# Kernel tuning notes

Hardware: AMD Instinct MI355X
Metric: run time of the kernel (lower is better)

The kernel has to match this reference:

```python
import jax, jax.numpy as jnp
import numpy as np

N_DYADIC = 0  # dyadic refinement order 'n' from SigLoss_MMD.__init__


def _sig_gram(X, Y, n):
    """Gram matrix of signature kernels k(x_i, y_j) via the first-order
    finite-difference PDE scheme used by sig_kernels_f/fb_mmd:
        K[i+1,j+1] = K[i+1,j] + K[i,j+1] + K[i,j]*(<dx_i, dy_j> - 1)
    with dyadically refined increments dx = (x_{t+1}-x_t)/2^n repeated 2^n times.
    X: (A, M, D), Y: (B, N, D) -> returns (A, B) = K[:, :, -1, -1].
    The row recurrence is a cumulative sum, so each PDE row is one cumsum
    (fully vectorized over all (A,B) pairs); lax.scan runs over rows.
    """
    f = 2 ** n
    incX = jnp.repeat((X[:, 1:] - X[:, :-1]) / f, f, axis=1)  # (A, MM, D)
    incY = jnp.repeat((Y[:, 1:] - Y[:, :-1]) / f, f, axis=1)  # (B, NN, D)
    Mmat = jnp.einsum('aid,bjd->abij', incX, incY)            # (A, B, MM, NN)
    A, B, MM, NN = Mmat.shape
    ones_col = jnp.ones((A, B, 1), Mmat.dtype)
    row0 = jnp.ones((A, B, NN + 1), Mmat.dtype)               # K[0, :] = 1

    def step(prev_row, Mrow):  # prev_row: (A,B,NN+1), Mrow: (A,B,NN)
        # K[i+1,j+1] - K[i+1,j] = K[i,j+1] + K[i,j]*(M[i,j]-1)  -> cumsum
        inc = prev_row[..., 1:] + prev_row[..., :-1] * (Mrow - 1.0)
        new_row = jnp.concatenate([ones_col, 1.0 + jnp.cumsum(inc, axis=-1)], axis=-1)
        return new_row, None

    last_row, _ = jax.lax.scan(step, row0, jnp.moveaxis(Mmat, 2, 0))
    return last_row[..., -1]  # (A, B)


def setup_inputs() -> dict:
    key = jax.random.key(0)
    kx, ky = jax.random.split(key)
    A, M, D = 64, 128, 128
    SCALE = 0.025  # keeps increment inner products small so the PDE stays bounded
    X = SCALE * jax.random.normal(kx, (A, M, D), dtype=jnp.float32)
    Y = SCALE * jax.random.normal(ky, (A, M, D), dtype=jnp.float32)
    return {"X": X, "Y": Y}


def reference(X, Y):
    K_XX = _sig_gram(X, X, N_DYADIC)
    K_YY = _sig_gram(Y, Y, N_DYADIC)
    K_XY = _sig_gram(X, Y, N_DYADIC)
    mmd_squared = jnp.mean(K_XX) + jnp.mean(K_YY) - 2.0 * jnp.mean(K_XY)
    return mmd_squared
```

## Files before the change

kernel.cpp:

```cpp
#include <hip/hip_runtime.h>
#include <hip/hip_bf16.h>

#define MM 127
#define CHUNK_U16 4096
#define MAT_U16   16384
#define ARR_U16   1048576
#define QS_STRIDE 136
#define QS_DWORDS (64 * QS_STRIDE)

typedef __attribute__((ext_vector_type(8))) short short8;
typedef __attribute__((ext_vector_type(4))) float floatx4;

__device__ __forceinline__ unsigned int pack_bf16_rne(float a, float b) {
  float2 rr; rr.x = a; rr.y = b;
  __hip_bfloat162 hp = __float22bfloat162_rn(rr);
  unsigned int hu; __builtin_memcpy(&hu, &hp, 4);
  return hu;
}

__device__ __forceinline__ void gload_lds16(const void* g, void* l) {
  __builtin_amdgcn_global_load_lds(
      (const __attribute__((address_space(1))) unsigned int*)g,
      (__attribute__((address_space(3))) unsigned int*)l, 16, 0, 0);
}

__device__ __forceinline__ float wave_shr1(float x) {
  return __int_as_float(__builtin_amdgcn_update_dpp(
      0, __float_as_int(x), 0x138, 0xf, 0xf, true));
}

__global__ __launch_bounds__(256) void prep_kernel(
    const float* __restrict__ X, const float* __restrict__ Y,
    unsigned short* __restrict__ base, float* __restrict__ acc)
{
  if (blockIdx.x == 0 && threadIdx.x == 0) acc[0] = 0.f;
  const int bid = blockIdx.x;
  const int c = bid & 3;
  const int m = (bid >> 2) & 63;
  const int isY = bid >> 8;
  const float* src = (isY ? Y : X) + m * 128 * 128;
  unsigned short* dst = base + isY * ARR_U16 + m * MAT_U16 + c * CHUNK_U16;

  for (int s = threadIdx.x; s < 512; s += 256) {
    const int r = s >> 2;
    const int g = (s & 3) ^ ((r >> 1) & 3);
    uint4 hv = make_uint4(0, 0, 0, 0);
    if (r < MM) {
      const float* p = src + r * 128 + c * 32 + g * 8;
      float4 u0 = *reinterpret_cast<const float4*>(p);
      float4 u1 = *reinterpret_cast<const float4*>(p + 4);
      float4 v0 = *reinterpret_cast<const float4*>(p + 128);
      float4 v1 = *reinterpret_cast<const float4*>(p + 132);
      hv.x = pack_bf16_rne(v0.x - u0.x, v0.y - u0.y);
      hv.y = pack_bf16_rne(v0.z - u0.z, v0.w - u0.w);
      hv.z = pack_bf16_rne(v1.x - u1.x, v1.y - u1.y);
      hv.w = pack_bf16_rne(v1.z - u1.z, v1.w - u1.w);
    }
    *reinterpret_cast<uint4*>(dst + s * 8) = hv;
  }
}

__global__ __launch_bounds__(256, 4) void sig_pair_kernel(
    const unsigned short* __restrict__ base, float* __restrict__ acc)
{
  __shared__ unsigned int smw[QS_DWORDS];
  unsigned short* const sm = reinterpret_cast<unsigned short*>(smw);
  const int tid = threadIdx.x;
  const int bid = blockIdx.x;

  float w;
  int a, b, srcA, srcB;
  if (bid < 4160) {
    int p = bid;
    srcA = 0;
    if (p >= 2080) { p -= 2080; srcA = 1; }
    srcB = srcA;
    int ia = (int)((sqrtf(8.0f * (float)p + 1.0f) - 1.0f) * 0.5f);
    while ((ia + 1) * (ia + 2) / 2 <= p) ia++;
    while (ia * (ia + 1) / 2 > p) ia--;
    int ib = p - ia * (ia + 1) / 2;
    a = ia; b = ib;
    w = (a == b ? 1.0f : 2.0f) / 4096.0f;
  } else {
    int p = bid - 4160;
    a = p >> 6; b = p & 63;
    srcA = 0; srcB = 1;
    w = -2.0f / 4096.0f;
  }
  const unsigned short* Am = base + srcA * ARR_U16 + a * MAT_U16;
  const unsigned short* Bm = base + srcB * ARR_U16 + b * MAT_U16;

  const int wid = tid >> 6, lane = tid & 63;
  const int row0 = (wid >> 1) * 64, col0 = (wid & 1) * 64;
  const int lrow = lane & 15, quad = lane >> 4;

  const unsigned short* gp = ((wid < 2) ? Am : Bm) + (wid & 1) * 2048 + lane * 8;
  const unsigned int dq = wid * 2048;

  floatx4 acc4[4][4];
#pragma unroll
  for (int tr = 0; tr < 4; ++tr)
#pragma unroll
    for (int tc = 0; tc < 4; ++tc) acc4[tr][tc] = (floatx4){0.f, 0.f, 0.f, 0.f};

#pragma unroll
  for (int s = 0; s < 4; ++s)
    gload_lds16(gp + s * 512, &sm[dq + s * 512]);

  for (int c = 0; c < 4; ++c) {
    __syncthreads();
    if (c < 3) {
      const unsigned short* g = gp + (c + 1) * CHUNK_U16;
      const unsigned int db_ = ((c + 1) & 1) * 8192 + dq;
#pragma unroll
      for (int s = 0; s < 4; ++s)
        gload_lds16(g + s * 512, &sm[db_ + s * 512]);
    }
    const unsigned int bb = (c & 1) * 8192;
    short8 bh[4];
#pragma unroll
    for (int tc = 0; tc < 4; ++tc) {
      int r = col0 + tc * 16 + lrow;
      int off = r * 32 + ((quad ^ ((r >> 1) & 3)) * 8);
      bh[tc] = *reinterpret_cast<const short8*>(&sm[bb + 4096 + off]);
    }
#pragma unroll
    for (int tr = 0; tr < 4; ++tr) {
      int r = row0 + tr * 16 + lrow;
      int off = r * 32 + ((quad ^ ((r >> 1) & 3)) * 8);
      short8 ah = *reinterpret_cast<const short8*>(&sm[bb + off]);
#pragma unroll
      for (int tc = 0; tc < 4; ++tc)
        acc4[tr][tc] = __builtin_amdgcn_mfma_f32_16x16x32_bf16(ah, bh[tc], acc4[tr][tc], 0, 0, 0);
    }
  }
  __syncthreads();

  {
    uint4 z = make_uint4(0u, 0u, 0u, 0u);
    uint4* smw4 = reinterpret_cast<uint4*>(smw);
    for (int i = tid; i < QS_DWORDS / 4; i += 256) smw4[i] = z;
  }
  __syncthreads();

#pragma unroll
  for (int tr = 0; tr < 4; ++tr) {
    const int im0 = row0 + tr * 16 + quad * 4;
#pragma unroll
    for (int tc = 0; tc < 4; ++tc) {
      const int jm = col0 + tc * 16 + lrow;
      if (jm < MM) {
        const int lt = (jm + 1) >> 1;
        const int half = (jm & 1) ? 0 : 1;
        const int phys0 = im0 + jm + 5 - 4 * (lt >> 1) - 4 * (lt & 1);
        unsigned short* p = &sm[(lt * QS_STRIDE + phys0) * 2 + half];
        unsigned int u01 = pack_bf16_rne(acc4[tr][tc][0], acc4[tr][tc][1]);
        unsigned int u23 = pack_bf16_rne(acc4[tr][tc][2], acc4[tr][tc][3]);
        p[0] = (unsigned short)u01;
        p[2] = (unsigned short)(u01 >> 16);
        p[4] = (unsigned short)u23;
        if (im0 + 3 < MM) p[6] = (unsigned short)(u23 >> 16);
      }
    }
  }
  __syncthreads();

  if (wid == ((bid >> 8) & 3)) {
    const int l = lane;
    const int shift = 4 * (l >> 1) + 4 * (l & 1) - 4;
    const unsigned int lbase = l * QS_STRIDE;

    auto loadg = [&](int g) -> uint4 {
      int pb = 4 * g - shift;
      pb = pb < 0 ? 132 : (pb > 128 ? 128 : pb);
      return *reinterpret_cast<const uint4*>(&smw[lbase + pb]);
    };

    float curE = 1.f, curO = 1.f;
    float npE = (l == 0) ? 0.f : 1.f, npO = 1.f;
    uint4 P0 = loadg(0), P1 = loadg(1), P2 = loadg(2);

    for (int g = 0; g < 63; ++g) {
      const uint4 cur = P0;
      P0 = P1; P1 = P2;
      if (g < 61) P2 = loadg(g + 3);
      unsigned int uu[4] = {cur.x, cur.y, cur.z, cur.w};
#pragma unroll
      for (int e = 0; e < 4; ++e) {
        unsigned int u = uu[e];
        float mE = __uint_as_float(u << 16) - 1.0f;
        float mO = __uint_as_float(u & 0xFFFF0000u) - 1.0f;
        float ncE = wave_shr1(curO);
        float ncO = curE;
        float vE = (curE + npE * mE) + ncE;
        float vO = (curO + npO * mO) + ncO;
        npE = ncE; npO = ncO;
        curE = vE; curO = vO;
      }
    }
    {
      unsigned int uu[2] = {P0.x, P0.y};
#pragma unroll
      for (int e = 0; e < 2; ++e) {
        unsigned int u = uu[e];
        float mE = __uint_as_float(u << 16) - 1.0f;
        float mO = __uint_as_float(u & 0xFFFF0000u) - 1.0f;
        float ncE = wave_shr1(curO);
        float ncO = curE;
        float vE = (curE + npE * mE) + ncE;
        float vO = (curO + npO * mO) + ncO;
        npE = ncE; npO = ncO;
        curE = vE; curO = vO;
      }
    }
    if (l == 63) atomicAdd(acc, w * curO);
  }
}

__global__ void finalize_kernel(const float* __restrict__ acc,
                                unsigned int* __restrict__ out) {
  float v = acc[0];
  __hip_bfloat16 bv = __float2bfloat16(v);
  unsigned short u;
  __builtin_memcpy(&u, &bv, sizeof(u));
  out[0] = ((unsigned int)u << 16) | (unsigned int)u;
}

extern "C" void kernel_launch(void* const* d_in, const int* in_sizes, int n_in,
                              void* d_out, int out_size, void* d_ws, size_t ws_size,
                              hipStream_t stream) {
  const float* X = (const float*)d_in[0];
  const float* Y = (const float*)d_in[1];
  float* acc = (float*)d_ws;
  unsigned short* base = (unsigned short*)((char*)d_ws + 1024);

  prep_kernel<<<512, 256, 0, stream>>>(X, Y, base, acc);
  sig_pair_kernel<<<8256, 256, 0, stream>>>(base, acc);
  finalize_kernel<<<1, 1, 0, stream>>>(acc, (unsigned int*)d_out);
}
```

Measured before the change: 187.3 us.

## Load MFMA operands directly from global memory instead of staging through LDS

```diff
diff --git a/kernel.cpp b/kernel.cpp
--- a/kernel.cpp
+++ b/kernel.cpp
@@ -16,12 +16,6 @@
   __hip_bfloat162 hp = __float22bfloat162_rn(rr);
   unsigned int hu; __builtin_memcpy(&hu, &hp, 4);
   return hu;
-}
-
-__device__ __forceinline__ void gload_lds16(const void* g, void* l) {
-  __builtin_amdgcn_global_load_lds(
-      (const __attribute__((address_space(1))) unsigned int*)g,
-      (__attribute__((address_space(3))) unsigned int*)l, 16, 0, 0);
 }
 
 __device__ __forceinline__ float wave_shr1(float x) {
@@ -94,52 +88,38 @@
   const int row0 = (wid >> 1) * 64, col0 = (wid & 1) * 64;
   const int lrow = lane & 15, quad = lane >> 4;
 
-  const unsigned short* gp = ((wid < 2) ? Am : Bm) + (wid & 1) * 2048 + lane * 8;
-  const unsigned int dq = wid * 2048;
-
-  floatx4 acc4[4][4];
-#pragma unroll
-  for (int tr = 0; tr < 4; ++tr)
-#pragma unroll
-    for (int tc = 0; tc < 4; ++tc) acc4[tr][tc] = (floatx4){0.f, 0.f, 0.f, 0.f};
-
-#pragma unroll
-  for (int s = 0; s < 4; ++s)
-    gload_lds16(gp + s * 512, &sm[dq + s * 512]);
-
-  for (int c = 0; c < 4; ++c) {
-    __syncthreads();
-    if (c < 3) {
-      const unsigned short* g = gp + (c + 1) * CHUNK_U16;
-      const unsigned int db_ = ((c + 1) & 1) * 8192 + dq;
-#pragma unroll
-      for (int s = 0; s < 4; ++s)
-        gload_lds16(g + s * 512, &sm[db_ + s * 512]);
-    }
-    const unsigned int bb = (c & 1) * 8192;
-    short8 bh[4];
-#pragma unroll
-    for (int tc = 0; tc < 4; ++tc) {
-      int r = col0 + tc * 16 + lrow;
-      int off = r * 32 + ((quad ^ ((r >> 1) & 3)) * 8);
-      bh[tc] = *reinterpret_cast<const short8*>(&sm[bb + 4096 + off]);
-    }
-#pragma unroll
-    for (int tr = 0; tr < 4; ++tr) {
-      int r = row0 + tr * 16 + lrow;
-      int off = r * 32 + ((quad ^ ((r >> 1) & 3)) * 8);
-      short8 ah = *reinterpret_cast<const short8*>(&sm[bb + off]);
-#pragma unroll
-      for (int tc = 0; tc < 4; ++tc)
-        acc4[tr][tc] = __builtin_amdgcn_mfma_f32_16x16x32_bf16(ah, bh[tc], acc4[tr][tc], 0, 0, 0);
-    }
-  }
-  __syncthreads();
-
   {
     uint4 z = make_uint4(0u, 0u, 0u, 0u);
     uint4* smw4 = reinterpret_cast<uint4*>(smw);
     for (int i = tid; i < QS_DWORDS / 4; i += 256) smw4[i] = z;
+  }
+
+  floatx4 acc4[4][4];
+#pragma unroll
+  for (int tr = 0; tr < 4; ++tr)
+#pragma unroll
+    for (int tc = 0; tc < 4; ++tc) acc4[tr][tc] = (floatx4){0.f, 0.f, 0.f, 0.f};
+
+#pragma unroll 1
+  for (int c = 0; c < 4; ++c) {
+    const unsigned short* Ac = Am + c * CHUNK_U16;
+    const unsigned short* Bc = Bm + c * CHUNK_U16;
+    short8 bh[4];
+#pragma unroll
+    for (int tc = 0; tc < 4; ++tc) {
+      int r = col0 + tc * 16 + lrow;
+      int off = r * 32 + ((quad ^ ((r >> 1) & 3)) * 8);
+      bh[tc] = *reinterpret_cast<const short8*>(&Bc[off]);
+    }
+#pragma unroll
+    for (int tr = 0; tr < 4; ++tr) {
+      int r = row0 + tr * 16 + lrow;
+      int off = r * 32 + ((quad ^ ((r >> 1) & 3)) * 8);
+      short8 ah = *reinterpret_cast<const short8*>(&Ac[off]);
+#pragma unroll
+      for (int tc = 0; tc < 4; ++tc)
+        acc4[tr][tc] = __builtin_amdgcn_mfma_f32_16x16x32_bf16(ah, bh[tc], acc4[tr][tc], 0, 0, 0);
+    }
   }
   __syncthreads();
 
@@ -178,12 +158,12 @@
 
     float curE = 1.f, curO = 1.f;
     float npE = (l == 0) ? 0.f : 1.f, npO = 1.f;
-    uint4 P0 = loadg(0), P1 = loadg(1), P2 = loadg(2);
+    uint4 P0 = loadg(0), P1 = loadg(1);
 
     for (int g = 0; g < 63; ++g) {
       const uint4 cur = P0;
-      P0 = P1; P1 = P2;
-      if (g < 61) P2 = loadg(g + 3);
+      P0 = P1;
+      if (g < 62) P1 = loadg(g + 2);
       unsigned int uu[4] = {cur.x, cur.y, cur.z, cur.w};
 #pragma unroll
       for (int e = 0; e < 4; ++e) {
```

Result: no change. 189.4 us (+1.1%).
